# Kernel tuning notes

Measured on AMD Instinct MI355X. Metric: run time of the kernel, lower is better.

## Reference

```python
import jax, jax.numpy as jnp
import numpy as np

N_LAYERS = 24  # number of recurrent applications of the shared HashLinear


def setup_inputs() -> dict:
    key = jax.random.key(0)
    ks = jax.random.split(key, 9)
    B, D_IN, N, N_OUT = 1024, 784, 4096, 10
    s_in = 1.0 / np.sqrt(D_IN)
    s_h = 1.0 / np.sqrt(N)
    x = jax.random.normal(ks[0], (B, D_IN), jnp.float32)
    # nn.Linear(prod(input_dim), 2*n_units)
    W_in = jax.random.uniform(ks[1], (2 * N, D_IN), jnp.float32, -s_in, s_in)
    b_in = jax.random.uniform(ks[2], (2 * N,), jnp.float32, -s_in, s_in)
    # HashLinear(n_units, n_units, period=1, 'hash'): learnable +/-1 context key + shared linear
    key_sp = jnp.where(jax.random.bernoulli(ks[3], 0.5, (1, N)), 1.0, -1.0).astype(jnp.float32)
    W_sp = jax.random.uniform(ks[4], (N, N), jnp.float32, -s_h, s_h)
    b_sp = jax.random.uniform(ks[5], (N,), jnp.float32, -s_h, s_h)
    # HashLinear(n_units, 10, period=1, 'hash')
    key_f = jnp.where(jax.random.bernoulli(ks[6], 0.5, (1, N)), 1.0, -1.0).astype(jnp.float32)
    W_f = jax.random.uniform(ks[7], (N_OUT, N), jnp.float32, -s_h, s_h)
    b_f = jax.random.uniform(ks[8], (N_OUT,), jnp.float32, -s_h, s_h)
    return {"x": x, "W_in": W_in, "b_in": b_in, "key_sp": key_sp, "W_sp": W_sp,
            "b_sp": b_sp, "key_f": key_f, "W_f": W_f, "b_f": b_f, "time": 0}


def _hash_linear(xa, xb, o, W, b):
    # Superposition HashLinear: same shared weight applied to both streams,
    # each modulated by the +/-1 context key o ([n_in]).
    ya = (xa * o) @ W.T + b
    yb = (xb * o) @ W.T + b
    return ya, yb


def reference(x, W_in, b_in, key_sp, W_sp, b_sp, key_f, W_f, b_f, time):
    N = W_sp.shape[0]
    r = x @ W_in.T + b_in                 # [B, 2N]
    r_a, r_b = r[:, :N], r[:, N:]         # torch.split(r, n_units, 1)
    pre0 = r_a
    r_a, r_b = jax.nn.relu(r_a), jax.nn.relu(r_b)
    o = key_sp[time % key_sp.shape[0]]    # period=1, time=0 in the module

    def step(carry, _):
        a, b2 = carry
        ya, yb = _hash_linear(a, b2, o, W_sp, b_sp)
        return (jax.nn.relu(ya), jax.nn.relu(yb)), ya  # collect preactivation r_a

    (r_a, r_b), pres = jax.lax.scan(step, (r_a, r_b), None, length=N_LAYERS)
    of = key_f[time % key_f.shape[0]]
    out_a, out_b = _hash_linear(r_a, r_b, of, W_f, b_f)  # [B,10], [B,10]
    preactivations = jnp.concatenate([pre0[None], pres], axis=0)  # [N_LAYERS+1, B, N]
    return (out_a, out_b, preactivations)
```

## Files before the change

### kernel.cpp

```cpp
#include <hip/hip_runtime.h>
#include <hip/hip_bf16.h>
#include <stdint.h>

typedef __bf16 bf16x8 __attribute__((ext_vector_type(8)));
typedef float  f32x4  __attribute__((ext_vector_type(4)));

#define NH      4096
#define MB      1024
#define M2      2048
#define DIN     784
#define KPAD    832
#define N_IN    8192
#define NLAYERS 24
#define NOUT    10

#define ASLOT   (256 * 64)
#define BSLOT   (128 * 64)
#define SLOT    (ASLOT + BSLOT)

__device__ __forceinline__ unsigned short f2bf(float x) {
  union { float f; unsigned u; } v; v.f = x;
  unsigned r = v.u + 0x7FFFu + ((v.u >> 16) & 1u);
  return (unsigned short)(r >> 16);
}
__device__ __forceinline__ float bf2f(unsigned short u) {
  union { unsigned u; float f; } v; v.u = ((unsigned)u) << 16; return v.f;
}

__device__ __forceinline__ void async16(const void* g, void* l) {
  __builtin_amdgcn_global_load_lds(
      (const __attribute__((address_space(1))) void*)g,
      (__attribute__((address_space(3))) void*)l, 16, 0, 0);
}

__global__ void k_conv_wsp(const float* __restrict__ W, const float* __restrict__ o,
                           unsigned short* __restrict__ out) {
  size_t i = ((size_t)blockIdx.x * blockDim.x + threadIdx.x) * 4;
  if (i >= (size_t)NH * NH) return;
  float4 w = *reinterpret_cast<const float4*>(W + i);
  int k = (int)(i & (NH - 1));
  float4 ov = *reinterpret_cast<const float4*>(o + k);
  ushort4 r;
  r.x = f2bf(w.x * ov.x); r.y = f2bf(w.y * ov.y);
  r.z = f2bf(w.z * ov.z); r.w = f2bf(w.w * ov.w);
  *reinterpret_cast<ushort4*>(out + i) = r;
}

__global__ void k_conv_pad(const float* __restrict__ in, unsigned short* __restrict__ out,
                           int rows, int kin, int kout) {
  size_t i = (size_t)blockIdx.x * blockDim.x + threadIdx.x;
  if (i >= (size_t)rows * kout) return;
  int r = (int)(i / kout), c = (int)(i % kout);
  out[i] = (c < kin) ? f2bf(in[(size_t)r * kin + c]) : (unsigned short)0;
}

__device__ __forceinline__ void gemm_core(
    const unsigned short* __restrict__ Ag, const unsigned short* __restrict__ Bg,
    int K, int bm, int bn, unsigned short* lds, f32x4 acc[4][4])
{
  const int t    = threadIdx.x;
  const int lane = t & 63;
  const int wave = t >> 6;
  const int wm   = wave >> 1;
  const int wn   = wave & 1;
  const int l15  = lane & 15;
  const int lkb  = (lane >> 4) * 16;

  unsigned aG[4]; int aL[4];
#pragma unroll
  for (int j = 0; j < 4; ++j) {
    const int c   = j * 512 + t;
    const int row = c >> 3;
    const int sb  = ((c & 7) * 16) ^ ((row & 7) << 4);
    aL[j] = c * 8;
    aG[j] = (unsigned)((bm + row) * K + (sb >> 1));
  }
  unsigned bG[2]; int bL[2];
#pragma unroll
  for (int j = 0; j < 2; ++j) {
    const int c   = j * 512 + t;
    const int row = c >> 3;
    const int sb  = ((c & 7) * 16) ^ ((row & 7) << 4);
    bL[j] = c * 8;
    bG[j] = (unsigned)((bn + row) * K + (sb >> 1));
  }

  int aRd[2][4], bRd[2][4];
#pragma unroll
  for (int kk = 0; kk < 2; ++kk)
#pragma unroll
    for (int i = 0; i < 4; ++i) {
      const int ra = wm * 64 + i * 16 + l15;
      aRd[kk][i] = (ra * 128 + ((kk * 64 + lkb) ^ ((ra & 7) << 4))) >> 1;
      const int rb = wn * 64 + i * 16 + l15;
      bRd[kk][i] = (rb * 128 + ((kk * 64 + lkb) ^ ((rb & 7) << 4))) >> 1;
    }

  auto STAGE = [&](int slotIdx, int k0) {
    unsigned short* s = lds + slotIdx * SLOT;
#pragma unroll
    for (int j = 0; j < 4; ++j) async16(Ag + aG[j] + (unsigned)k0, s + aL[j]);
#pragma unroll
    for (int j = 0; j < 2; ++j) async16(Bg + bG[j] + (unsigned)k0, s + ASLOT + bL[j]);
  };

  const int nt = K >> 6;
  STAGE(0, 0);
  if (nt > 1) STAGE(1, 64);

  int s0 = 0;
  int s2 = 2;
  for (int kt = 0; kt < nt; ++kt) {
    __builtin_amdgcn_sched_barrier(0);
    if (kt + 1 < nt) asm volatile("s_waitcnt vmcnt(6)" ::: "memory");
    else             asm volatile("s_waitcnt vmcnt(0)" ::: "memory");
    __builtin_amdgcn_s_barrier();
    __builtin_amdgcn_sched_barrier(0);
    __builtin_amdgcn_s_setprio(1);
    if (kt + 2 < nt) STAGE(s2, (kt + 2) << 6);
    const unsigned short* base = lds + s0 * SLOT;
#pragma unroll
    for (int kk = 0; kk < 2; ++kk) {
      bf16x8 af[4], bv[4];
#pragma unroll
      for (int i = 0; i < 4; ++i) af[i] = *reinterpret_cast<const bf16x8*>(base + aRd[kk][i]);
#pragma unroll
      for (int i = 0; i < 4; ++i) bv[i] = *reinterpret_cast<const bf16x8*>(base + ASLOT + bRd[kk][i]);
#pragma unroll
      for (int mi = 0; mi < 4; ++mi)
#pragma unroll
        for (int ni = 0; ni < 4; ++ni)
          acc[mi][ni] = __builtin_amdgcn_mfma_f32_16x16x32_bf16(af[mi], bv[ni], acc[mi][ni], 0, 0, 0);
    }
    __builtin_amdgcn_s_setprio(0);
    s0 = (s0 == 2) ? 0 : s0 + 1;
    s2 = (s2 == 2) ? 0 : s2 + 1;
  }
}

__global__ __launch_bounds__(512, 2) void k_gemm_layer(
    const unsigned short* __restrict__ A, const unsigned short* __restrict__ W,
    const float* __restrict__ bias, float* __restrict__ preact,
    unsigned short* __restrict__ Anext)
{
  __shared__ __align__(16) unsigned short lds[3 * SLOT];
  const int bid = blockIdx.x;
  const int s   = ((bid & 7) << 5) + (bid >> 3);
  const int bm = (s >> 5) * 256;
  const int bn = (s & 31) * 128;
  f32x4 acc[4][4] = {};
  gemm_core(A, W, NH, bm, bn, lds, acc);

  const int lane = threadIdx.x & 63;
  const int wave = threadIdx.x >> 6;
  const int wm = (wave >> 1) * 64, wn = (wave & 1) * 64;
  const int l15 = lane & 15;
#pragma unroll
  for (int mi = 0; mi < 4; ++mi) {
    const int gm0 = bm + wm + mi * 16 + (lane >> 4) * 4;
#pragma unroll
    for (int ni = 0; ni < 4; ++ni) {
      const int gn = bn + wn + ni * 16 + l15;
      const float bv = bias[gn];
#pragma unroll
      for (int r = 0; r < 4; ++r) {
        const int gm = gm0 + r;
        const float y = acc[mi][ni][r] + bv;
        if (gm < MB) preact[(size_t)gm * NH + gn] = y;
        Anext[(size_t)gm * NH + gn] = f2bf(y > 0.f ? y : 0.f);
      }
    }
  }
}

__global__ __launch_bounds__(512, 2) void k_gemm_in(
    const unsigned short* __restrict__ X, const unsigned short* __restrict__ W,
    const float* __restrict__ bias, float* __restrict__ preact0,
    unsigned short* __restrict__ A0)
{
  __shared__ __align__(16) unsigned short lds[3 * SLOT];
  const int bid = blockIdx.x;
  const int s   = ((bid & 7) << 5) + (bid >> 3);
  const int bm = (s >> 6) * 256;
  const int bn = (s & 63) * 128;
  f32x4 acc[4][4] = {};
  gemm_core(X, W, KPAD, bm, bn, lds, acc);

  const int lane = threadIdx.x & 63;
  const int wave = threadIdx.x >> 6;
  const int wm = (wave >> 1) * 64, wn = (wave & 1) * 64;
  const int l15 = lane & 15;
#pragma unroll
  for (int mi = 0; mi < 4; ++mi) {
    const int gm0 = bm + wm + mi * 16 + (lane >> 4) * 4;
#pragma unroll
    for (int ni = 0; ni < 4; ++ni) {
      const int gn = bn + wn + ni * 16 + l15;
      const float bv = bias[gn];
#pragma unroll
      for (int r = 0; r < 4; ++r) {
        const int gm = gm0 + r;
        const float y = acc[mi][ni][r] + bv;
        const unsigned short rl = f2bf(y > 0.f ? y : 0.f);
        if (gn < NH) {
          preact0[(size_t)gm * NH + gn] = y;
          A0[(size_t)gm * NH + gn] = rl;
        } else {
          A0[(size_t)(MB + gm) * NH + (gn - NH)] = rl;
        }
      }
    }
  }
}

__global__ void k_final(const unsigned short* __restrict__ A,
                        const float* __restrict__ Wf, const float* __restrict__ of,
                        const float* __restrict__ bf_, float* __restrict__ out)
{
  const int m = blockIdx.x;
  const int t = threadIdx.x;
  float accj[NOUT] = {};
  for (int k = t; k < NH; k += 256) {
    const float a = bf2f(A[(size_t)m * NH + k]) * of[k];
#pragma unroll
    for (int j = 0; j < NOUT; ++j) accj[j] += a * Wf[j * NH + k];
  }
  __shared__ float red[4][NOUT];
#pragma unroll
  for (int j = 0; j < NOUT; ++j) {
    float v = accj[j];
    for (int off = 32; off > 0; off >>= 1) v += __shfl_down(v, off);
    if ((t & 63) == 0) red[t >> 6][j] = v;
  }
  __syncthreads();
  if (t < NOUT) {
    const float s = red[0][t] + red[1][t] + red[2][t] + red[3][t] + bf_[t];
    out[(size_t)m * NOUT + t] = s;
  }
}

extern "C" void kernel_launch(void* const* d_in, const int* in_sizes, int n_in,
                              void* d_out, int out_size, void* d_ws, size_t ws_size,
                              hipStream_t stream) {
  const float* x     = (const float*)d_in[0];
  const float* W_in  = (const float*)d_in[1];
  const float* b_in  = (const float*)d_in[2];
  const float* keysp = (const float*)d_in[3];
  const float* W_sp  = (const float*)d_in[4];
  const float* b_sp  = (const float*)d_in[5];
  const float* keyf  = (const float*)d_in[6];
  const float* W_f   = (const float*)d_in[7];
  const float* b_f   = (const float*)d_in[8];

  float* out    = (float*)d_out;
  float* preact = out + (size_t)2 * MB * NOUT;

  char* ws = (char*)d_ws;
  unsigned short* Wsp_bf = (unsigned short*)ws;  ws += (size_t)NH * NH * 2;
  unsigned short* A0     = (unsigned short*)ws;  ws += (size_t)M2 * NH * 2;
  unsigned short* A1     = (unsigned short*)ws;  ws += (size_t)M2 * NH * 2;
  unsigned short* Win_bf = (unsigned short*)ws;  ws += (size_t)N_IN * KPAD * 2;
  unsigned short* X_bf   = (unsigned short*)ws;  ws += (size_t)MB * KPAD * 2;

  k_conv_wsp<<<(NH * (size_t)NH / 4 + 255) / 256, 256, 0, stream>>>(W_sp, keysp, Wsp_bf);
  k_conv_pad<<<((size_t)N_IN * KPAD + 255) / 256, 256, 0, stream>>>(W_in, Win_bf, N_IN, DIN, KPAD);
  k_conv_pad<<<((size_t)MB * KPAD + 255) / 256, 256, 0, stream>>>(x, X_bf, MB, DIN, KPAD);

  k_gemm_in<<<256, 512, 0, stream>>>(X_bf, Win_bf, b_in, preact, A0);

  unsigned short* Ain = A0;
  unsigned short* Aout = A1;
  for (int tlay = 0; tlay < NLAYERS; ++tlay) {
    float* pre = preact + (size_t)(tlay + 1) * MB * NH;
    k_gemm_layer<<<256, 512, 0, stream>>>(Ain, Wsp_bf, b_sp, pre, Aout);
    unsigned short* tmp = Ain; Ain = Aout; Aout = tmp;
  }

  k_final<<<M2, 256, 0, stream>>>(Ain, W_f, keyf, b_f, out);
}
```

Baseline: 1.758 ms.

## Split K across wave groups with 128x64 per-wave tiles and LDS reduction

Reorganizes the GEMM so the 8 waves form two K-groups that alternate k-tiles. Each wave now computes a 128x64 sub-tile with 8x4 MFMA accumulators, which raises fragment reuse per LDS read. The two partial sums are then reduced through LDS, and only the first four waves run the epilogue. In exchange, register use doubles, which at launch bounds (512,2) may cause spills or lower occupancy, and it adds a reduction pass plus idle waves during every other k-step.

```diff
diff --git a/kernel.cpp b/kernel.cpp
--- a/kernel.cpp
+++ b/kernel.cpp
@@ -56,53 +56,39 @@
 
 __device__ __forceinline__ void gemm_core(
     const unsigned short* __restrict__ Ag, const unsigned short* __restrict__ Bg,
-    int K, int bm, int bn, unsigned short* lds, f32x4 acc[4][4])
+    int K, int bm, int bn, unsigned short* lds, f32x4 acc[8][4])
 {
   const int t    = threadIdx.x;
   const int lane = t & 63;
   const int wave = t >> 6;
-  const int wm   = wave >> 1;
-  const int wn   = wave & 1;
+  const int kg   = wave >> 2;
+  const int qm   = (wave >> 1) & 1;
+  const int qn   = wave & 1;
   const int l15  = lane & 15;
   const int lkb  = (lane >> 4) * 16;
 
-  unsigned aG[4]; int aL[4];
-#pragma unroll
-  for (int j = 0; j < 4; ++j) {
-    const int c   = j * 512 + t;
-    const int row = c >> 3;
-    const int sb  = ((c & 7) * 16) ^ ((row & 7) << 4);
-    aL[j] = c * 8;
-    aG[j] = (unsigned)((bm + row) * K + (sb >> 1));
-  }
-  unsigned bG[2]; int bL[2];
-#pragma unroll
-  for (int j = 0; j < 2; ++j) {
-    const int c   = j * 512 + t;
-    const int row = c >> 3;
-    const int sb  = ((c & 7) * 16) ^ ((row & 7) << 4);
-    bL[j] = c * 8;
-    bG[j] = (unsigned)((bn + row) * K + (sb >> 1));
-  }
-
-  int aRd[2][4], bRd[2][4];
-#pragma unroll
-  for (int kk = 0; kk < 2; ++kk)
-#pragma unroll
-    for (int i = 0; i < 4; ++i) {
-      const int ra = wm * 64 + i * 16 + l15;
-      aRd[kk][i] = (ra * 128 + ((kk * 64 + lkb) ^ ((ra & 7) << 4))) >> 1;
-      const int rb = wn * 64 + i * 16 + l15;
-      bRd[kk][i] = (rb * 128 + ((kk * 64 + lkb) ^ ((rb & 7) << 4))) >> 1;
-    }
+  const int srow = t >> 3;
+  const int sb   = ((t & 7) * 16) ^ ((srow & 7) << 4);
+  const unsigned aG0 = (unsigned)((bm + srow) * K + (sb >> 1));
+  const unsigned bG0 = (unsigned)((bn + srow) * K + (sb >> 1));
 
   auto STAGE = [&](int slotIdx, int k0) {
     unsigned short* s = lds + slotIdx * SLOT;
 #pragma unroll
-    for (int j = 0; j < 4; ++j) async16(Ag + aG[j] + (unsigned)k0, s + aL[j]);
-#pragma unroll
-    for (int j = 0; j < 2; ++j) async16(Bg + bG[j] + (unsigned)k0, s + ASLOT + bL[j]);
+    for (int j = 0; j < 4; ++j)
+      async16(Ag + aG0 + (unsigned)(j * 64 * K + k0), s + t * 8 + j * 4096);
+#pragma unroll
+    for (int j = 0; j < 2; ++j)
+      async16(Bg + bG0 + (unsigned)(j * 64 * K + k0), s + ASLOT + t * 8 + j * 4096);
   };
+
+  const int swz = (l15 & 7) << 4;
+  int aB[2], bB[2];
+#pragma unroll
+  for (int kk = 0; kk < 2; ++kk) {
+    aB[kk] = ((qm * 128 + l15) * 128 + ((kk * 64 + lkb) ^ swz)) >> 1;
+    bB[kk] = ((qn * 64  + l15) * 128 + ((kk * 64 + lkb) ^ swz)) >> 1;
+  }
 
   const int nt = K >> 6;
   STAGE(0, 0);
@@ -116,25 +102,47 @@
     else             asm volatile("s_waitcnt vmcnt(0)" ::: "memory");
     __builtin_amdgcn_s_barrier();
     __builtin_amdgcn_sched_barrier(0);
-    __builtin_amdgcn_s_setprio(1);
     if (kt + 2 < nt) STAGE(s2, (kt + 2) << 6);
-    const unsigned short* base = lds + s0 * SLOT;
-#pragma unroll
-    for (int kk = 0; kk < 2; ++kk) {
-      bf16x8 af[4], bv[4];
-#pragma unroll
-      for (int i = 0; i < 4; ++i) af[i] = *reinterpret_cast<const bf16x8*>(base + aRd[kk][i]);
-#pragma unroll
-      for (int i = 0; i < 4; ++i) bv[i] = *reinterpret_cast<const bf16x8*>(base + ASLOT + bRd[kk][i]);
-#pragma unroll
-      for (int mi = 0; mi < 4; ++mi)
-#pragma unroll
-        for (int ni = 0; ni < 4; ++ni)
-          acc[mi][ni] = __builtin_amdgcn_mfma_f32_16x16x32_bf16(af[mi], bv[ni], acc[mi][ni], 0, 0, 0);
-    }
-    __builtin_amdgcn_s_setprio(0);
+    if (((kt ^ kg) & 1) == 0) {
+      __builtin_amdgcn_s_setprio(1);
+      const unsigned short* base = lds + s0 * SLOT;
+#pragma unroll
+      for (int kk = 0; kk < 2; ++kk) {
+        bf16x8 af[8], bv[4];
+#pragma unroll
+        for (int i = 0; i < 8; ++i)
+          af[i] = *reinterpret_cast<const bf16x8*>(base + aB[kk] + i * 1024);
+#pragma unroll
+        for (int i = 0; i < 4; ++i)
+          bv[i] = *reinterpret_cast<const bf16x8*>(base + ASLOT + bB[kk] + i * 1024);
+#pragma unroll
+        for (int mi = 0; mi < 8; ++mi)
+#pragma unroll
+          for (int ni = 0; ni < 4; ++ni)
+            acc[mi][ni] = __builtin_amdgcn_mfma_f32_16x16x32_bf16(af[mi], bv[ni], acc[mi][ni], 0, 0, 0);
+      }
+      __builtin_amdgcn_s_setprio(0);
+    }
     s0 = (s0 == 2) ? 0 : s0 + 1;
     s2 = (s2 == 2) ? 0 : s2 + 1;
+  }
+
+  float* fl = (float*)lds;
+  const int q = qm * 2 + qn;
+  const int mbase = q * 8192 + lane * 128;
+  __syncthreads();
+  if (kg == 1) {
+#pragma unroll
+    for (int i = 0; i < 32; ++i)
+      *reinterpret_cast<f32x4*>(fl + mbase + (((i * 16) ^ ((lane & 7) << 4)) >> 2)) = acc[i >> 2][i & 3];
+  }
+  __syncthreads();
+  if (kg == 0) {
+#pragma unroll
+    for (int i = 0; i < 32; ++i) {
+      f32x4 v = *reinterpret_cast<const f32x4*>(fl + mbase + (((i * 16) ^ ((lane & 7) << 4)) >> 2));
+      acc[i >> 2][i & 3] += v;
+    }
   }
 }
 
@@ -148,19 +156,20 @@
   const int s   = ((bid & 7) << 5) + (bid >> 3);
   const int bm = (s >> 5) * 256;
   const int bn = (s & 31) * 128;
-  f32x4 acc[4][4] = {};
+  f32x4 acc[8][4] = {};
   gemm_core(A, W, NH, bm, bn, lds, acc);
 
   const int lane = threadIdx.x & 63;
   const int wave = threadIdx.x >> 6;
-  const int wm = (wave >> 1) * 64, wn = (wave & 1) * 64;
+  if ((wave >> 2) != 0) return;
+  const int qm = (wave >> 1) & 1, qn = wave & 1;
   const int l15 = lane & 15;
 #pragma unroll
-  for (int mi = 0; mi < 4; ++mi) {
-    const int gm0 = bm + wm + mi * 16 + (lane >> 4) * 4;
+  for (int mi = 0; mi < 8; ++mi) {
+    const int gm0 = bm + qm * 128 + mi * 16 + (lane >> 4) * 4;
 #pragma unroll
     for (int ni = 0; ni < 4; ++ni) {
-      const int gn = bn + wn + ni * 16 + l15;
+      const int gn = bn + qn * 64 + ni * 16 + l15;
       const float bv = bias[gn];
 #pragma unroll
       for (int r = 0; r < 4; ++r) {
@@ -183,19 +192,20 @@
   const int s   = ((bid & 7) << 5) + (bid >> 3);
   const int bm = (s >> 6) * 256;
   const int bn = (s & 63) * 128;
-  f32x4 acc[4][4] = {};
+  f32x4 acc[8][4] = {};
   gemm_core(X, W, KPAD, bm, bn, lds, acc);
 
   const int lane = threadIdx.x & 63;
   const int wave = threadIdx.x >> 6;
-  const int wm = (wave >> 1) * 64, wn = (wave & 1) * 64;
+  if ((wave >> 2) != 0) return;
+  const int qm = (wave >> 1) & 1, qn = wave & 1;
   const int l15 = lane & 15;
 #pragma unroll
-  for (int mi = 0; mi < 4; ++mi) {
-    const int gm0 = bm + wm + mi * 16 + (lane >> 4) * 4;
+  for (int mi = 0; mi < 8; ++mi) {
+    const int gm0 = bm + qm * 128 + mi * 16 + (lane >> 4) * 4;
 #pragma unroll
     for (int ni = 0; ni < 4; ++ni) {
-      const int gn = bn + wn + ni * 16 + l15;
+      const int gn = bn + qn * 64 + ni * 16 + l15;
       const float bv = bias[gn];
 #pragma unroll
       for (int r = 0; r < 4; ++r) {
```

New measurement: 1.985 ms. 12.9% more time.

## Software-pipeline LDS fragment reads against MFMA in GEMM main loop

Applied to the files above, without the earlier changes.

Restructures the K loop so that LDS reads for the next half-tile (and the first half of the next K tile) are issued before the MFMAs on the current fragments. This double-buffers the register fragments and moves the barrier between the two MFMA halves, so LDS latency is hidden behind matrix math. It also simplifies the async staging address computation to a single base plus strided offsets. The cost is more live registers (two fragment sets) and a reordered barrier, which could hurt occupancy at 512 threads with 2 blocks per CU.

```diff
diff --git a/kernel.cpp b/kernel.cpp
--- a/kernel.cpp
+++ b/kernel.cpp
@@ -66,24 +66,20 @@
   const int l15  = lane & 15;
   const int lkb  = (lane >> 4) * 16;
 
-  unsigned aG[4]; int aL[4];
-#pragma unroll
-  for (int j = 0; j < 4; ++j) {
-    const int c   = j * 512 + t;
-    const int row = c >> 3;
-    const int sb  = ((c & 7) * 16) ^ ((row & 7) << 4);
-    aL[j] = c * 8;
-    aG[j] = (unsigned)((bm + row) * K + (sb >> 1));
-  }
-  unsigned bG[2]; int bL[2];
-#pragma unroll
-  for (int j = 0; j < 2; ++j) {
-    const int c   = j * 512 + t;
-    const int row = c >> 3;
-    const int sb  = ((c & 7) * 16) ^ ((row & 7) << 4);
-    bL[j] = c * 8;
-    bG[j] = (unsigned)((bn + row) * K + (sb >> 1));
-  }
+  const int srow = t >> 3;
+  const int sb   = ((t & 7) * 16) ^ ((srow & 7) << 4);
+  const unsigned aG0 = (unsigned)((bm + srow) * K + (sb >> 1));
+  const unsigned bG0 = (unsigned)((bn + srow) * K + (sb >> 1));
+
+  auto STAGE = [&](int slotIdx, int k0) {
+    unsigned short* s = lds + slotIdx * SLOT;
+#pragma unroll
+    for (int j = 0; j < 4; ++j)
+      async16(Ag + aG0 + (unsigned)(j * 64 * K + k0), s + t * 8 + j * 4096);
+#pragma unroll
+    for (int j = 0; j < 2; ++j)
+      async16(Bg + bG0 + (unsigned)(j * 64 * K + k0), s + ASLOT + t * 8 + j * 4096);
+  };
 
   int aRd[2][4], bRd[2][4];
 #pragma unroll
@@ -96,45 +92,51 @@
       bRd[kk][i] = (rb * 128 + ((kk * 64 + lkb) ^ ((rb & 7) << 4))) >> 1;
     }
 
-  auto STAGE = [&](int slotIdx, int k0) {
-    unsigned short* s = lds + slotIdx * SLOT;
-#pragma unroll
-    for (int j = 0; j < 4; ++j) async16(Ag + aG[j] + (unsigned)k0, s + aL[j]);
-#pragma unroll
-    for (int j = 0; j < 2; ++j) async16(Bg + bG[j] + (unsigned)k0, s + ASLOT + bL[j]);
+  bf16x8 aX[4], bX[4], aY[4], bY[4];
+
+  auto READS = [&](int slotIdx, int kk, bf16x8* A4, bf16x8* B4) {
+    const unsigned short* base = lds + slotIdx * SLOT;
+#pragma unroll
+    for (int i = 0; i < 4; ++i) A4[i] = *reinterpret_cast<const bf16x8*>(base + aRd[kk][i]);
+#pragma unroll
+    for (int i = 0; i < 4; ++i) B4[i] = *reinterpret_cast<const bf16x8*>(base + ASLOT + bRd[kk][i]);
+  };
+  auto MM = [&](const bf16x8* A4, const bf16x8* B4) {
+    __builtin_amdgcn_s_setprio(1);
+#pragma unroll
+    for (int mi = 0; mi < 4; ++mi)
+#pragma unroll
+      for (int ni = 0; ni < 4; ++ni)
+        acc[mi][ni] = __builtin_amdgcn_mfma_f32_16x16x32_bf16(A4[mi], B4[ni], acc[mi][ni], 0, 0, 0);
+    __builtin_amdgcn_s_setprio(0);
   };
 
   const int nt = K >> 6;
   STAGE(0, 0);
-  if (nt > 1) STAGE(1, 64);
-
-  int s0 = 0;
-  int s2 = 2;
+  STAGE(1, 64);
+  asm volatile("s_waitcnt vmcnt(6)" ::: "memory");
+  __builtin_amdgcn_s_barrier();
+  __builtin_amdgcn_sched_barrier(0);
+  READS(0, 0, aX, bX);
+
+  int s0 = 0, s1 = 1, s2 = 2;
   for (int kt = 0; kt < nt; ++kt) {
+    if (kt + 2 < nt) STAGE(s2, (kt + 2) << 6);
+    READS(s0, 1, aY, bY);
+    MM(aX, bX);
     __builtin_amdgcn_sched_barrier(0);
-    if (kt + 1 < nt) asm volatile("s_waitcnt vmcnt(6)" ::: "memory");
-    else             asm volatile("s_waitcnt vmcnt(0)" ::: "memory");
-    __builtin_amdgcn_s_barrier();
+    asm volatile("s_waitcnt lgkmcnt(0)" ::: "memory");
     __builtin_amdgcn_sched_barrier(0);
-    __builtin_amdgcn_s_setprio(1);
-    if (kt + 2 < nt) STAGE(s2, (kt + 2) << 6);
-    const unsigned short* base = lds + s0 * SLOT;
-#pragma unroll
-    for (int kk = 0; kk < 2; ++kk) {
-      bf16x8 af[4], bv[4];
-#pragma unroll
-      for (int i = 0; i < 4; ++i) af[i] = *reinterpret_cast<const bf16x8*>(base + aRd[kk][i]);
-#pragma unroll
-      for (int i = 0; i < 4; ++i) bv[i] = *reinterpret_cast<const bf16x8*>(base + ASLOT + bRd[kk][i]);
-#pragma unroll
-      for (int mi = 0; mi < 4; ++mi)
-#pragma unroll
-        for (int ni = 0; ni < 4; ++ni)
-          acc[mi][ni] = __builtin_amdgcn_mfma_f32_16x16x32_bf16(af[mi], bv[ni], acc[mi][ni], 0, 0, 0);
-    }
-    __builtin_amdgcn_s_setprio(0);
-    s0 = (s0 == 2) ? 0 : s0 + 1;
-    s2 = (s2 == 2) ? 0 : s2 + 1;
+    if (kt + 1 < nt) {
+      if (kt + 2 < nt) asm volatile("s_waitcnt vmcnt(6)" ::: "memory");
+      else             asm volatile("s_waitcnt vmcnt(0)" ::: "memory");
+      __builtin_amdgcn_s_barrier();
+      __builtin_amdgcn_sched_barrier(0);
+      READS(s1, 0, aX, bX);
+    }
+    MM(aY, bY);
+    const int n0 = s1, n1 = s2, n2 = s0;
+    s0 = n0; s1 = n1; s2 = n2;
   }
 }
 
```

New measurement: 1.670 ms. 1.05x faster.
